# Kernel optimization log

Measured on AMD Instinct MI355X. Metric: run time of the kernel, lower is better.

The kernel has to match this reference:

```python
import jax, jax.numpy as jnp
import numpy as np

B, N, DIM, H, DK, DV = 2, 2048, 1536, 8, 64, 192


def relative_shift(x):
    # x: [b, h, t1, 2*t1-1] -> [b, h, t1, t1] via Transformer-XL pad/reshape trick
    b, h, t1, t2 = x.shape
    x = jnp.pad(x, ((0, 0), (0, 0), (0, 0), (1, 0)))  # prepend zero column
    t2p = t2 + 1
    x = x.reshape(b, h, t2p, t1)
    x = x[:, :, 1:, :].reshape(b, h, t1, t2)
    return x[..., : (t2p + 1) // 2]


def setup_inputs() -> dict:
    key = jax.random.key(0)
    ks = jax.random.split(key, 9)
    s = 0.02
    return {
        "x": jax.random.normal(ks[0], (B, N, DIM), jnp.float32),
        "Wq": jax.random.normal(ks[1], (DIM, H * DK), jnp.float32) * s,
        "Wk": jax.random.normal(ks[2], (DIM, H * DK), jnp.float32) * s,
        "Wv": jax.random.normal(ks[3], (DIM, H * DV), jnp.float32) * s,
        "W_rel": jax.random.normal(ks[4], (1, H * DK), jnp.float32) * s,
        "Wo": jax.random.normal(ks[5], (H * DV, DIM), jnp.float32) * s,
        "bo": jnp.zeros((DIM,), jnp.float32),
        "rel_content_bias": jax.random.normal(ks[6], (1, H, 1, DK), jnp.float32),
        "rel_pos_bias": jax.random.normal(ks[7], (1, H, 1, DK), jnp.float32),
    }


def reference(x, Wq, Wk, Wv, W_rel, Wo, bo, rel_content_bias, rel_pos_bias):
    b, n, _ = x.shape
    scale = DK ** -0.5
    split = lambda t, d: t.reshape(b, n, H, d).transpose(0, 2, 1, 3)  # b h n d
    q = split(x @ Wq, DK) * scale
    k = split(x @ Wk, DK)
    v = split(x @ Wv, DV)

    content_logits = jnp.einsum("bhid,bhjd->bhij", q + rel_content_bias, k)

    distances = jnp.arange(-n + 1, n, dtype=jnp.float32)[:, None]  # [2n-1, 1]
    rel_k = (distances @ W_rel).reshape(2 * n - 1, H, DK).transpose(1, 0, 2)  # h j d
    rel_logits = jnp.einsum("bhid,hjd->bhij", q + rel_pos_bias, rel_k)
    rel_logits = relative_shift(rel_logits)

    attn = jax.nn.softmax(content_logits + rel_logits, axis=-1)
    out = jnp.einsum("bhij,bhjd->bhid", attn, v)
    out = out.transpose(0, 2, 1, 3).reshape(b, n, H * DV)
    return out @ Wo + bo
```

## Files before the change

### kernel.cpp

```cpp
#include <hip/hip_runtime.h>
#include <math.h>

typedef __attribute__((ext_vector_type(8))) short short8;
typedef __attribute__((ext_vector_type(4))) float floatx4;

namespace {
constexpr int kB = 2, kN = 2048, kDIM = 1536, kH = 8, kDK = 64, kDV = 192;
constexpr int kHDV = kH * kDV;
constexpr float kScale = 0.125f;
}

__device__ __forceinline__ unsigned short f2b(float f) {
    union { float f; unsigned u; } v; v.f = f;
    unsigned r = (v.u + 0x7FFFu + ((v.u >> 16) & 1u)) >> 16;
    return (unsigned short)r;
}

__global__ __launch_bounds__(256) void conv_w(
    const float* __restrict__ src, unsigned short* __restrict__ dst, int Ncols)
{
    __shared__ float Ts[32][33];
    const int tx = threadIdx.x & 31, ty = threadIdx.x >> 5;
    const int k0 = blockIdx.x * 32, n0 = blockIdx.y * 32;
#pragma unroll
    for (int p = 0; p < 4; ++p)
        Ts[ty + p * 8][tx] = src[(size_t)(k0 + ty + p * 8) * Ncols + n0 + tx];
    __syncthreads();
#pragma unroll
    for (int p = 0; p < 4; ++p)
        dst[(size_t)(n0 + ty + p * 8) * kDIM + k0 + tx] = f2b(Ts[tx][ty + p * 8]);
}

__global__ __launch_bounds__(256) void conv_x(
    const float* __restrict__ x, unsigned short* __restrict__ xb)
{
    int idx = blockIdx.x * 256 + threadIdx.x;
    float4 v = *(const float4*)&x[(size_t)idx * 4];
    ushort4 o; o.x = f2b(v.x); o.y = f2b(v.y); o.z = f2b(v.z); o.w = f2b(v.w);
    *(ushort4*)&xb[(size_t)idx * 4] = o;
}

__global__ __launch_bounds__(256) void wcm_pre(
    const float* __restrict__ Wq, const float* __restrict__ Wrel,
    const float* __restrict__ rpb, float* __restrict__ wcm)
{
    int gid = blockIdx.x * 256 + threadIdx.x;
    if (gid < 12288) {
        int dim = gid >> 3, h = gid & 7;
        float s = 0.f;
#pragma unroll 8
        for (int d = 0; d < 64; ++d)
            s += Wq[(size_t)dim * 512 + h * 64 + d] * Wrel[h * 64 + d];
        wcm[h * kDIM + dim] = s * kScale;
    } else if (gid < 12296) {
        int h = gid - 12288;
        float s = 0.f;
#pragma unroll 8
        for (int d = 0; d < 64; ++d) s += rpb[h * 64 + d] * Wrel[h * 64 + d];
        wcm[12288 + h] = s;
    }
}

__global__ __launch_bounds__(256) void c_gemm(
    const float* __restrict__ x, const float* __restrict__ wcm,
    float* __restrict__ cw)
{
    const int row  = blockIdx.x * 4 + (threadIdx.x >> 6);
    const int lane = threadIdx.x & 63;
    const float* xr = x + (size_t)row * kDIM;

    float4 xv[6];
#pragma unroll
    for (int c = 0; c < 6; ++c)
        xv[c] = *(const float4*)&xr[c * 256 + lane * 4];

    float acc[8];
#pragma unroll
    for (int h = 0; h < 8; ++h) {
        const float* wr = wcm + h * kDIM;
        float a = 0.f;
#pragma unroll
        for (int c = 0; c < 6; ++c) {
            float4 wv = *(const float4*)&wr[c * 256 + lane * 4];
            a += xv[c].x * wv.x + xv[c].y * wv.y + xv[c].z * wv.z + xv[c].w * wv.w;
        }
        acc[h] = a;
    }
#pragma unroll
    for (int h = 0; h < 8; ++h) {
        float a = acc[h];
        a += __shfl_xor(a, 1, 64);
        a += __shfl_xor(a, 2, 64);
        a += __shfl_xor(a, 4, 64);
        a += __shfl_xor(a, 8, 64);
        a += __shfl_xor(a, 16, 64);
        a += __shfl_xor(a, 32, 64);
        acc[h] = a;
    }
    if (lane == 0) {
        const int b = row >> 11, i = row & 2047;
#pragma unroll
        for (int h = 0; h < 8; ++h)
            cw[(size_t)(b * 8 + h) * kN + i] = acc[h] + wcm[12288 + h];
    }
}

__global__ __launch_bounds__(256) void mm_qkv(
    const unsigned short* __restrict__ xb,
    const unsigned short* __restrict__ wt,
    const float* __restrict__ rcb,
    unsigned short* __restrict__ qo,
    unsigned short* __restrict__ ko,
    unsigned short* __restrict__ vo)
{
    __shared__ unsigned short A_lds[128 * 72];
    __shared__ unsigned short B_lds[128 * 72];
    const int tid = threadIdx.x;
    const int wave = tid >> 6, lane = tid & 63, lm = lane & 15, lg = lane >> 4;
    const int bm = blockIdx.y * 128, bn = blockIdx.x * 128;
    const int mb = (wave >> 1) * 64, nb = (wave & 1) * 64;

    floatx4 acc[4][4];
#pragma unroll
    for (int i = 0; i < 4; ++i)
#pragma unroll
        for (int j = 0; j < 4; ++j)
#pragma unroll
            for (int r = 0; r < 4; ++r) acc[i][j][r] = 0.f;

    const int srow = tid >> 3, scc = (tid & 7) * 8;
    short8 ra[4], rb[4];
#pragma unroll
    for (int p = 0; p < 4; ++p) {
        ra[p] = *(const short8*)&xb[(size_t)(bm + srow + p * 32) * kDIM + scc];
        rb[p] = *(const short8*)&wt[(size_t)(bn + srow + p * 32) * kDIM + scc];
    }

    for (int kt = 0; kt < 24; ++kt) {
        __syncthreads();
#pragma unroll
        for (int p = 0; p < 4; ++p) {
            *(short8*)&A_lds[(srow + p * 32) * 72 + scc] = ra[p];
            *(short8*)&B_lds[(srow + p * 32) * 72 + scc] = rb[p];
        }
        __syncthreads();
        if (kt < 23) {
            int k0 = (kt + 1) * 64;
#pragma unroll
            for (int p = 0; p < 4; ++p) {
                ra[p] = *(const short8*)&xb[(size_t)(bm + srow + p * 32) * kDIM + k0 + scc];
                rb[p] = *(const short8*)&wt[(size_t)(bn + srow + p * 32) * kDIM + k0 + scc];
            }
        }
#pragma unroll
        for (int ks = 0; ks < 2; ++ks) {
            short8 af[4], bf[4];
#pragma unroll
            for (int mi = 0; mi < 4; ++mi)
                af[mi] = *(const short8*)&A_lds[(mb + mi * 16 + lm) * 72 + lg * 8 + 32 * ks];
#pragma unroll
            for (int ni = 0; ni < 4; ++ni)
                bf[ni] = *(const short8*)&B_lds[(nb + ni * 16 + lm) * 72 + lg * 8 + 32 * ks];
#pragma unroll
            for (int mi = 0; mi < 4; ++mi)
#pragma unroll
                for (int ni = 0; ni < 4; ++ni)
                    acc[mi][ni] = __builtin_amdgcn_mfma_f32_16x16x32_bf16(
                        af[mi], bf[ni], acc[mi][ni], 0, 0, 0);
        }
    }

#pragma unroll
    for (int mi = 0; mi < 4; ++mi)
#pragma unroll
        for (int ni = 0; ni < 4; ++ni)
#pragma unroll
            for (int r = 0; r < 4; ++r) {
                int row = bm + mb + mi * 16 + lg * 4 + r;
                int b = row >> 11, i = row & 2047;
                int col = bn + nb + ni * 16 + lm;
                float v = acc[mi][ni][r];
                if (bn < 512) {
                    int h = col >> 6, d = col & 63;
                    qo[((size_t)(b * 8 + h) * kN + i) * kDK + d] =
                        f2b(v * kScale + rcb[h * 64 + d]);
                } else if (bn < 1024) {
                    int c2 = col - 512, h = c2 >> 6, d = c2 & 63;
                    ko[((size_t)(b * 8 + h) * kN + i) * kDK + d] = f2b(v);
                } else {
                    int c2 = col - 1024, h = c2 / 192, d = c2 - h * 192;
                    vo[((size_t)(b * 8 + h) * kN + i) * kDV + d] = f2b(v);
                }
            }
}

__global__ __launch_bounds__(256) void vtrans(
    const unsigned short* __restrict__ vw, unsigned short* __restrict__ vt)
{
    __shared__ unsigned short Ts[32][33];
    const int tx = threadIdx.x & 31, ty = threadIdx.x >> 5;
    const int i0 = blockIdx.x * 32, d0 = blockIdx.y * 32, bh = blockIdx.z;
#pragma unroll
    for (int p = 0; p < 4; ++p)
        Ts[ty + p * 8][tx] = vw[((size_t)bh * kN + i0 + ty + p * 8) * kDV + d0 + tx];
    __syncthreads();
#pragma unroll
    for (int p = 0; p < 4; ++p)
        vt[((size_t)bh * kDV + d0 + ty + p * 8) * kN + i0 + tx] = Ts[tx][ty + p * 8];
}

__global__ __launch_bounds__(256) void flash_attn(
    const unsigned short* __restrict__ q,
    const unsigned short* __restrict__ k,
    const unsigned short* __restrict__ vt,
    const float* __restrict__ crel,
    unsigned short* __restrict__ ao)
{
    __shared__ unsigned short K_lds[64 * 72];
    __shared__ unsigned short V_lds[192 * 72];
    __shared__ unsigned short P_lds[4 * 16 * 72];
    __shared__ float cs[64];

    const int tid = threadIdx.x;
    const int wave = tid >> 6, lane = tid & 63, lm = lane & 15, lg = lane >> 4;
    const int bh = blockIdx.y;
    const int i0 = blockIdx.x * 64;

    short8 qA[2];
    {
        const size_t qb = ((size_t)bh * kN + i0 + wave * 16 + lm) * kDK + lg * 8;
        qA[0] = *(const short8*)&q[qb];
        qA[1] = *(const short8*)&q[qb + 32];
    }
    if (tid < 64) cs[tid] = crel[(size_t)bh * kN + i0 + tid];

    floatx4 o4[12];
#pragma unroll
    for (int nd = 0; nd < 12; ++nd)
#pragma unroll
        for (int r = 0; r < 4; ++r) o4[nd][r] = 0.f;
    float m_[4] = {-INFINITY, -INFINITY, -INFINITY, -INFINITY};
    float l_[4] = {0.f, 0.f, 0.f, 0.f};

    const unsigned short* kb = k + (size_t)bh * kN * kDK;
    const unsigned short* vb = vt + (size_t)bh * kDV * kN;
    const int pbase = wave * 16 * 72;

    for (int t = 0; t < 32; ++t) {
        const int j0 = t * 64;
        __syncthreads();
#pragma unroll
        for (int p = 0; p < 2; ++p) {
            int c = tid + p * 256;
            int row = c >> 3, cc = (c & 7) * 8;
            *(short8*)&K_lds[row * 72 + cc] =
                *(const short8*)&kb[(size_t)(j0 + row) * kDK + cc];
        }
#pragma unroll
        for (int p = 0; p < 6; ++p) {
            int c = tid + p * 256;
            int row = c >> 3, cc = (c & 7) * 8;
            *(short8*)&V_lds[row * 72 + cc] =
                *(const short8*)&vb[(size_t)row * kN + j0 + cc];
        }
        __syncthreads();

        floatx4 s4[4];
#pragma unroll
        for (int st = 0; st < 4; ++st) {
#pragma unroll
            for (int r = 0; r < 4; ++r) s4[st][r] = 0.f;
#pragma unroll
            for (int ks = 0; ks < 2; ++ks) {
                short8 kf = *(const short8*)&K_lds[(st * 16 + lm) * 72 + lg * 8 + 32 * ks];
                s4[st] = __builtin_amdgcn_mfma_f32_16x16x32_bf16(qA[ks], kf, s4[st], 0, 0, 0);
            }
        }

        float alpha[4];
#pragma unroll
        for (int r = 0; r < 4; ++r) {
            const int lrow = wave * 16 + lg * 4 + r;
            const float ci = cs[lrow];
            const float gi = (float)(i0 + lrow);
            float sv[4];
#pragma unroll
            for (int st = 0; st < 4; ++st)
                sv[st] = s4[st][r] + ((float)(j0 + st * 16 + lm) - gi) * ci;
            float mx = fmaxf(fmaxf(sv[0], sv[1]), fmaxf(sv[2], sv[3]));
            mx = fmaxf(mx, __shfl_xor(mx, 1, 64));
            mx = fmaxf(mx, __shfl_xor(mx, 2, 64));
            mx = fmaxf(mx, __shfl_xor(mx, 4, 64));
            mx = fmaxf(mx, __shfl_xor(mx, 8, 64));
            float mnew = fmaxf(m_[r], mx);
            alpha[r] = __expf(m_[r] - mnew);
            m_[r] = mnew;
            float ts = 0.f;
#pragma unroll
            for (int st = 0; st < 4; ++st) {
                float pv = __expf(sv[st] - mnew);
                ts += pv;
                P_lds[pbase + (lg * 4 + r) * 72 + st * 16 + lm] = f2b(pv);
            }
            ts += __shfl_xor(ts, 1, 64);
            ts += __shfl_xor(ts, 2, 64);
            ts += __shfl_xor(ts, 4, 64);
            ts += __shfl_xor(ts, 8, 64);
            l_[r] = l_[r] * alpha[r] + ts;
        }

#pragma unroll
        for (int nd = 0; nd < 12; ++nd)
#pragma unroll
            for (int r = 0; r < 4; ++r) o4[nd][r] *= alpha[r];

        short8 pa[2];
        pa[0] = *(const short8*)&P_lds[pbase + lm * 72 + lg * 8];
        pa[1] = *(const short8*)&P_lds[pbase + lm * 72 + lg * 8 + 32];
#pragma unroll
        for (int nd = 0; nd < 12; ++nd) {
#pragma unroll
            for (int ks = 0; ks < 2; ++ks) {
                short8 vf = *(const short8*)&V_lds[(nd * 16 + lm) * 72 + lg * 8 + 32 * ks];
                o4[nd] = __builtin_amdgcn_mfma_f32_16x16x32_bf16(pa[ks], vf, o4[nd], 0, 0, 0);
            }
        }
    }

    const int b = bh >> 3, h = bh & 7;
#pragma unroll
    for (int r = 0; r < 4; ++r) {
        float inv = 1.f / l_[r];
        size_t rowbase = ((size_t)b * kN + i0 + wave * 16 + lg * 4 + r) * (size_t)kHDV
                         + h * kDV;
#pragma unroll
        for (int nd = 0; nd < 12; ++nd)
            ao[rowbase + nd * 16 + lm] = f2b(o4[nd][r] * inv);
    }
}

__global__ __launch_bounds__(256) void mm_out(
    const unsigned short* __restrict__ aw,
    const unsigned short* __restrict__ wot,
    const float* __restrict__ bias,
    float* __restrict__ out)
{
    __shared__ unsigned short A_lds[128 * 72];
    __shared__ unsigned short B_lds[128 * 72];
    const int tid = threadIdx.x;
    const int wave = tid >> 6, lane = tid & 63, lm = lane & 15, lg = lane >> 4;
    const int bm = blockIdx.y * 128, bn = blockIdx.x * 128;
    const int mb = (wave >> 1) * 64, nb = (wave & 1) * 64;

    floatx4 acc[4][4];
#pragma unroll
    for (int i = 0; i < 4; ++i)
#pragma unroll
        for (int j = 0; j < 4; ++j)
#pragma unroll
            for (int r = 0; r < 4; ++r) acc[i][j][r] = 0.f;

    const int srow = tid >> 3, scc = (tid & 7) * 8;
    short8 ra[4], rb[4];
#pragma unroll
    for (int p = 0; p < 4; ++p) {
        ra[p] = *(const short8*)&aw[(size_t)(bm + srow + p * 32) * kDIM + scc];
        rb[p] = *(const short8*)&wot[(size_t)(bn + srow + p * 32) * kDIM + scc];
    }

    for (int kt = 0; kt < 24; ++kt) {
        __syncthreads();
#pragma unroll
        for (int p = 0; p < 4; ++p) {
            *(short8*)&A_lds[(srow + p * 32) * 72 + scc] = ra[p];
            *(short8*)&B_lds[(srow + p * 32) * 72 + scc] = rb[p];
        }
        __syncthreads();
        if (kt < 23) {
            int k0 = (kt + 1) * 64;
#pragma unroll
            for (int p = 0; p < 4; ++p) {
                ra[p] = *(const short8*)&aw[(size_t)(bm + srow + p * 32) * kDIM + k0 + scc];
                rb[p] = *(const short8*)&wot[(size_t)(bn + srow + p * 32) * kDIM + k0 + scc];
            }
        }
#pragma unroll
        for (int ks = 0; ks < 2; ++ks) {
            short8 af[4], bf[4];
#pragma unroll
            for (int mi = 0; mi < 4; ++mi)
                af[mi] = *(const short8*)&A_lds[(mb + mi * 16 + lm) * 72 + lg * 8 + 32 * ks];
#pragma unroll
            for (int ni = 0; ni < 4; ++ni)
                bf[ni] = *(const short8*)&B_lds[(nb + ni * 16 + lm) * 72 + lg * 8 + 32 * ks];
#pragma unroll
            for (int mi = 0; mi < 4; ++mi)
#pragma unroll
                for (int ni = 0; ni < 4; ++ni)
                    acc[mi][ni] = __builtin_amdgcn_mfma_f32_16x16x32_bf16(
                        af[mi], bf[ni], acc[mi][ni], 0, 0, 0);
        }
    }

#pragma unroll
    for (int mi = 0; mi < 4; ++mi)
#pragma unroll
        for (int ni = 0; ni < 4; ++ni)
#pragma unroll
            for (int r = 0; r < 4; ++r) {
                int row = bm + mb + mi * 16 + lg * 4 + r;
                int col = bn + nb + ni * 16 + lm;
                out[(size_t)row * kDIM + col] = acc[mi][ni][r] + bias[col];
            }
}

extern "C" void kernel_launch(void* const* d_in, const int* in_sizes, int n_in,
                              void* d_out, int out_size, void* d_ws, size_t ws_size,
                              hipStream_t stream)
{
    const float* x    = (const float*)d_in[0];
    const float* Wq   = (const float*)d_in[1];
    const float* Wk   = (const float*)d_in[2];
    const float* Wv   = (const float*)d_in[3];
    const float* Wrel = (const float*)d_in[4];
    const float* Wo   = (const float*)d_in[5];
    const float* bo   = (const float*)d_in[6];
    const float* rcb  = (const float*)d_in[7];
    const float* rpb  = (const float*)d_in[8];
    float* out = (float*)d_out;

    char* w = (char*)d_ws;
    unsigned short* xb  = (unsigned short*)(w);
    unsigned short* wt  = (unsigned short*)(w + 12582912);
    unsigned short* qw  = (unsigned short*)(w + 20447232);
    unsigned short* kw  = (unsigned short*)(w + 24641536);
    unsigned short* vw  = (unsigned short*)(w + 28835840);
    float*          cw  = (float*)(w + 41418752);
    float*          wcm = (float*)(w + 41549824);
    unsigned short* vtp = xb;
    unsigned short* awp = vw;
    unsigned short* wot = wt;

    { dim3 g(48, 16);  conv_w<<<g, 256, 0, stream>>>(Wq, wt,               512); }
    { dim3 g(48, 16);  conv_w<<<g, 256, 0, stream>>>(Wk, wt + 512  * 1536, 512); }
    { dim3 g(48, 48);  conv_w<<<g, 256, 0, stream>>>(Wv, wt + 1024 * 1536, 1536); }
    conv_x<<<6144, 256, 0, stream>>>(x, xb);
    wcm_pre<<<49, 256, 0, stream>>>(Wq, Wrel, rpb, wcm);
    c_gemm<<<1024, 256, 0, stream>>>(x, wcm, cw);

    { dim3 g(20, 32); mm_qkv<<<g, 256, 0, stream>>>(xb, wt, rcb, qw, kw, vw); }

    { dim3 g(48, 48); conv_w<<<g, 256, 0, stream>>>(Wo, wot, 1536); }
    { dim3 g(64, 6, 16); vtrans<<<g, 256, 0, stream>>>(vw, vtp); }

    { dim3 g(32, 16); flash_attn<<<g, 256, 0, stream>>>(qw, kw, vtp, cw, awp); }

    { dim3 g(12, 32); mm_out<<<g, 256, 0, stream>>>(awp, wot, bo, out); }
}
```

Measured before the change: 335.3 us.

## Prefetch K/V tiles into registers, use exp2 softmax, remap blocks, repad P

```diff
diff --git a/kernel.cpp b/kernel.cpp
--- a/kernel.cpp
+++ b/kernel.cpp
@@ -8,6 +8,7 @@
 constexpr int kB = 2, kN = 2048, kDIM = 1536, kH = 8, kDK = 64, kDV = 192;
 constexpr int kHDV = kH * kDV;
 constexpr float kScale = 0.125f;
+constexpr float kLog2e = 1.44269504088896340736f;
 }
 
 __device__ __forceinline__ unsigned short f2b(float f) {
@@ -51,13 +52,13 @@
 #pragma unroll 8
         for (int d = 0; d < 64; ++d)
             s += Wq[(size_t)dim * 512 + h * 64 + d] * Wrel[h * 64 + d];
-        wcm[h * kDIM + dim] = s * kScale;
+        wcm[h * kDIM + dim] = s * kScale * kLog2e;
     } else if (gid < 12296) {
         int h = gid - 12288;
         float s = 0.f;
 #pragma unroll 8
         for (int d = 0; d < 64; ++d) s += rpb[h * 64 + d] * Wrel[h * 64 + d];
-        wcm[12288 + h] = s;
+        wcm[12288 + h] = s * kLog2e;
     }
 }
 
@@ -183,7 +184,7 @@
                 if (bn < 512) {
                     int h = col >> 6, d = col & 63;
                     qo[((size_t)(b * 8 + h) * kN + i) * kDK + d] =
-                        f2b(v * kScale + rcb[h * 64 + d]);
+                        f2b((v * kScale + rcb[h * 64 + d]) * kLog2e);
                 } else if (bn < 1024) {
                     int c2 = col - 512, h = c2 >> 6, d = c2 & 63;
                     ko[((size_t)(b * 8 + h) * kN + i) * kDK + d] = f2b(v);
@@ -218,13 +219,15 @@
 {
     __shared__ unsigned short K_lds[64 * 72];
     __shared__ unsigned short V_lds[192 * 72];
-    __shared__ unsigned short P_lds[4 * 16 * 72];
+    __shared__ unsigned short P_lds[4 * 16 * 68];
     __shared__ float cs[64];
 
     const int tid = threadIdx.x;
     const int wave = tid >> 6, lane = tid & 63, lm = lane & 15, lg = lane >> 4;
-    const int bh = blockIdx.y;
-    const int i0 = blockIdx.x * 64;
+    const int id = blockIdx.x;
+    const int rem = id >> 3;
+    const int bh = (id & 7) * 2 + (rem >> 5);
+    const int i0 = (rem & 31) * 64;
 
     short8 qA[2];
     {
@@ -244,26 +247,36 @@
 
     const unsigned short* kb = k + (size_t)bh * kN * kDK;
     const unsigned short* vb = vt + (size_t)bh * kDV * kN;
-    const int pbase = wave * 16 * 72;
+    const int pbase = wave * 16 * 68;
+    const int srow = tid >> 3, scol = (tid & 7) * 8;
+
+    short8 rk[2], rv[6];
+#pragma unroll
+    for (int p = 0; p < 2; ++p)
+        rk[p] = *(const short8*)&kb[(size_t)(srow + p * 32) * kDK + scol];
+#pragma unroll
+    for (int p = 0; p < 6; ++p)
+        rv[p] = *(const short8*)&vb[(size_t)(srow + p * 32) * kN + scol];
 
     for (int t = 0; t < 32; ++t) {
         const int j0 = t * 64;
         __syncthreads();
 #pragma unroll
-        for (int p = 0; p < 2; ++p) {
-            int c = tid + p * 256;
-            int row = c >> 3, cc = (c & 7) * 8;
-            *(short8*)&K_lds[row * 72 + cc] =
-                *(const short8*)&kb[(size_t)(j0 + row) * kDK + cc];
-        }
-#pragma unroll
-        for (int p = 0; p < 6; ++p) {
-            int c = tid + p * 256;
-            int row = c >> 3, cc = (c & 7) * 8;
-            *(short8*)&V_lds[row * 72 + cc] =
-                *(const short8*)&vb[(size_t)row * kN + j0 + cc];
-        }
-        __syncthreads();
+        for (int p = 0; p < 2; ++p)
+            *(short8*)&K_lds[(srow + p * 32) * 72 + scol] = rk[p];
+#pragma unroll
+        for (int p = 0; p < 6; ++p)
+            *(short8*)&V_lds[(srow + p * 32) * 72 + scol] = rv[p];
+        __syncthreads();
+        if (t < 31) {
+            const int j1 = j0 + 64;
+#pragma unroll
+            for (int p = 0; p < 2; ++p)
+                rk[p] = *(const short8*)&kb[(size_t)(j1 + srow + p * 32) * kDK + scol];
+#pragma unroll
+            for (int p = 0; p < 6; ++p)
+                rv[p] = *(const short8*)&vb[(size_t)(srow + p * 32) * kN + j1 + scol];
+        }
 
         floatx4 s4[4];
 #pragma unroll
@@ -280,9 +293,9 @@
         float alpha[4];
 #pragma unroll
         for (int r = 0; r < 4; ++r) {
-            const int lrow = wave * 16 + lg * 4 + r;
-            const float ci = cs[lrow];
-            const float gi = (float)(i0 + lrow);
+            const int row = wave * 16 + lg * 4 + r;
+            const float ci = cs[row];
+            const float gi = (float)(i0 + row);
             float sv[4];
 #pragma unroll
             for (int st = 0; st < 4; ++st)
@@ -293,14 +306,14 @@
             mx = fmaxf(mx, __shfl_xor(mx, 4, 64));
             mx = fmaxf(mx, __shfl_xor(mx, 8, 64));
             float mnew = fmaxf(m_[r], mx);
-            alpha[r] = __expf(m_[r] - mnew);
+            alpha[r] = exp2f(m_[r] - mnew);
             m_[r] = mnew;
             float ts = 0.f;
 #pragma unroll
             for (int st = 0; st < 4; ++st) {
-                float pv = __expf(sv[st] - mnew);
+                float pv = exp2f(sv[st] - mnew);
                 ts += pv;
-                P_lds[pbase + (lg * 4 + r) * 72 + st * 16 + lm] = f2b(pv);
+                P_lds[pbase + (lg * 4 + r) * 68 + st * 16 + lm] = f2b(pv);
             }
             ts += __shfl_xor(ts, 1, 64);
             ts += __shfl_xor(ts, 2, 64);
@@ -315,8 +328,8 @@
             for (int r = 0; r < 4; ++r) o4[nd][r] *= alpha[r];
 
         short8 pa[2];
-        pa[0] = *(const short8*)&P_lds[pbase + lm * 72 + lg * 8];
-        pa[1] = *(const short8*)&P_lds[pbase + lm * 72 + lg * 8 + 32];
+        pa[0] = *(const short8*)&P_lds[pbase + lm * 68 + lg * 8];
+        pa[1] = *(const short8*)&P_lds[pbase + lm * 68 + lg * 8 + 32];
 #pragma unroll
         for (int nd = 0; nd < 12; ++nd) {
 #pragma unroll
@@ -453,7 +466,7 @@
     { dim3 g(48, 48); conv_w<<<g, 256, 0, stream>>>(Wo, wot, 1536); }
     { dim3 g(64, 6, 16); vtrans<<<g, 256, 0, stream>>>(vw, vtp); }
 
-    { dim3 g(32, 16); flash_attn<<<g, 256, 0, stream>>>(qw, kw, vtp, cw, awp); }
+    flash_attn<<<512, 256, 0, stream>>>(qw, kw, vtp, cw, awp);
 
     { dim3 g(12, 32); mm_out<<<g, 256, 0, stream>>>(awp, wot, bo, out); }
 }
```

Measured after the change: 339.4 us. Within noise of the previous version (+1.2%).
